# Performance work log

Measured on AMD Instinct MI355X. Metric: run time of the kernel, lower is better.

The kernel has to match this reference:

```python
import jax, jax.numpy as jnp
import numpy as np

B, T, IN, H, L, C = 64, 2048, 64, 128, 2, 8


def setup_inputs() -> dict:
    key = jax.random.key(0)
    ks = jax.random.split(key, 11)
    s = 1.0 / np.sqrt(H)  # torch nn.RNN default init scale
    return {
        "x": jax.random.normal(ks[0], (B, T, IN), dtype=jnp.float32),
        "W_ih0": jax.random.uniform(ks[1], (H, IN), jnp.float32, -s, s),
        "W_hh0": jax.random.uniform(ks[2], (H, H), jnp.float32, -s, s),
        "b_ih0": jax.random.uniform(ks[3], (H,), jnp.float32, -s, s),
        "b_hh0": jax.random.uniform(ks[4], (H,), jnp.float32, -s, s),
        "W_ih1": jax.random.uniform(ks[5], (H, H), jnp.float32, -s, s),
        "W_hh1": jax.random.uniform(ks[6], (H, H), jnp.float32, -s, s),
        "b_ih1": jax.random.uniform(ks[7], (H,), jnp.float32, -s, s),
        "b_hh1": jax.random.uniform(ks[8], (H,), jnp.float32, -s, s),
        "W_fc": jax.random.uniform(ks[9], (C, H), jnp.float32, -s, s),
        "b_fc": jax.random.uniform(ks[10], (C,), jnp.float32, -s, s),
    }


def _rnn_layer(x, W_ih, W_hh, b_ih, b_hh):
    # x: (B, T, D_in) -> (B, T, H); h0 = zeros (matches torch h0)
    # Precompute the input projection as one big GEMM outside the scan.
    x_proj = jnp.einsum('btd,hd->bth', x, W_ih) + b_ih + b_hh  # (B,T,H)
    x_proj_t = jnp.swapaxes(x_proj, 0, 1)  # (T,B,H)
    h0 = jnp.zeros((x.shape[0], W_hh.shape[0]), dtype=x.dtype)

    def step(h, xp):
        h_new = jnp.tanh(xp + h @ W_hh.T)
        return h_new, h_new

    _, hs = jax.lax.scan(step, h0, x_proj_t)  # (T,B,H)
    return jnp.swapaxes(hs, 0, 1)  # (B,T,H)


def reference(x, W_ih0, W_hh0, b_ih0, b_hh0, W_ih1, W_hh1, b_ih1, b_hh1, W_fc, b_fc):
    h1 = _rnn_layer(x, W_ih0, W_hh0, b_ih0, b_hh0)   # layer 0
    h2 = _rnn_layer(h1, W_ih1, W_hh1, b_ih1, b_hh1)  # layer 1
    logits = jnp.einsum('bth,ch->btc', h2, W_fc) + b_fc  # (B,T,C)
    return logits
```

## Files before the change

### kernel.cpp

```cpp
#include <hip/hip_runtime.h>

#define B_ 64
#define T_ 2048
#define IN_ 64
#define H_ 128
#define C_ 8

typedef _Float16 f16x2 __attribute__((ext_vector_type(2)));

__device__ __forceinline__ f16x2 pk(float a, float b) {
  f16x2 r; r.x = (_Float16)a; r.y = (_Float16)b; return r;
}
__device__ __forceinline__ f16x2 as_h2(int v) { return __builtin_bit_cast(f16x2, v); }

__device__ __forceinline__ float dot2(f16x2 a, f16x2 b, float c) {
#if __has_builtin(__builtin_amdgcn_fdot2)
  return __builtin_amdgcn_fdot2(a, b, c, false);
#else
  float r;
  asm("v_dot2_f32_f16 %0, %1, %2, %3" : "=v"(r) : "v"(a), "v"(b), "v"(c));
  return r;
#endif
}

__device__ __forceinline__ float tanh_fast(float x) {
  float e = __expf(2.0f * x);
  return 1.0f - 2.0f * __builtin_amdgcn_rcpf(e + 1.0f);
}

__device__ __forceinline__ float dpp_add_x1(float v) {
  return v + __int_as_float(__builtin_amdgcn_update_dpp(0, __float_as_int(v), 0xB1, 0xF, 0xF, true));
}
__device__ __forceinline__ float dpp_add_x2(float v) {
  return v + __int_as_float(__builtin_amdgcn_update_dpp(0, __float_as_int(v), 0x4E, 0xF, 0xF, true));
}
__device__ __forceinline__ float swz_add_x4(float v) {
  return v + __int_as_float(__builtin_amdgcn_ds_swizzle(__float_as_int(v), 0x101F));
}

__device__ __forceinline__ void block_sync_lds() {
  asm volatile("s_waitcnt lgkmcnt(0)" ::: "memory");
  __builtin_amdgcn_s_barrier();
  asm volatile("" ::: "memory");
}

#define DOT8(A, Q, W, BASE)            \
  A = dot2(as_h2(Q.x), W[BASE+0], A);  \
  A = dot2(as_h2(Q.y), W[BASE+1], A);  \
  A = dot2(as_h2(Q.z), W[BASE+2], A);  \
  A = dot2(as_h2(Q.w), W[BASE+3], A);

__global__ __launch_bounds__(256) void k_xproj(
    const float* __restrict__ x, const float* __restrict__ Wih0,
    const float* __restrict__ bih0, const float* __restrict__ bhh0,
    _Float16* __restrict__ xp) {
  __shared__ __align__(16) _Float16 xs[4][2][IN_];
  const int wave = threadIdx.x >> 6, lane = threadIdx.x & 63;
  const int gw = blockIdx.x * 4 + wave;
  const int ROWS = 32;
  const size_t r0 = (size_t)gw * ROWS;

  f16x2 wA[32], wB[32];
  const float2* W2 = (const float2*)Wih0;
#pragma unroll
  for (int p = 0; p < 32; ++p) {
    float2 a = W2[(lane * 2) * 32 + p];
    float2 b = W2[(lane * 2 + 1) * 32 + p];
    wA[p] = pk(a.x, a.y); wB[p] = pk(b.x, b.y);
  }
  const float ba = bih0[lane * 2] + bhh0[lane * 2];
  const float bb = bih0[lane * 2 + 1] + bhh0[lane * 2 + 1];

  xs[wave][0][lane] = (_Float16)x[r0 * IN_ + lane];
  float xn = x[(r0 + 1) * IN_ + lane];
  for (int rr = 0; rr < ROWS; ++rr) {
    const int buf = rr & 1;
    if (rr + 1 < ROWS) xs[wave][buf ^ 1][lane] = (_Float16)xn;
    if (rr + 2 < ROWS) xn = x[(r0 + rr + 2) * IN_ + lane];
    asm volatile("s_waitcnt lgkmcnt(0)" ::: "memory");
    const int4* xv = (const int4*)xs[wave][buf];
    int4 q0 = xv[0], q1 = xv[1], q2 = xv[2], q3 = xv[3];
    int4 q4 = xv[4], q5 = xv[5], q6 = xv[6], q7 = xv[7];
    float a0 = 0.f, a1 = 0.f, c0 = 0.f, c1 = 0.f;
    DOT8(a0, q0, wA, 0)  DOT8(c0, q0, wB, 0)
    DOT8(a1, q1, wA, 4)  DOT8(c1, q1, wB, 4)
    DOT8(a0, q2, wA, 8)  DOT8(c0, q2, wB, 8)
    DOT8(a1, q3, wA, 12) DOT8(c1, q3, wB, 12)
    DOT8(a0, q4, wA, 16) DOT8(c0, q4, wB, 16)
    DOT8(a1, q5, wA, 20) DOT8(c1, q5, wB, 20)
    DOT8(a0, q6, wA, 24) DOT8(c0, q6, wB, 24)
    DOT8(a1, q7, wA, 28) DOT8(c1, q7, wB, 28)
    *(f16x2*)&xp[(r0 + rr) * H_ + lane * 2] = pk(a0 + a1 + ba, c0 + c1 + bb);
  }
}

#define L0STEP(SS, XA, RI, WI)                                             \
  {                                                                        \
    block_sync_lds();                                                      \
    const int s_ = (SS);                                                   \
    if (s_ < T_) {                                                         \
      int4 q0 = hp[(RI) + rot0], q1 = hp[(RI) + rot1];                     \
      int4 q2 = hp[(RI) + rot2], q3 = hp[(RI) + rot3];                     \
      float a0 = 0.f, a1 = 0.f, c0 = 0.f, c1 = 0.f;                        \
      DOT8(a0, q0, wA, 0)  DOT8(c0, q0, wB, 0)                             \
      DOT8(a1, q1, wA, 4)  DOT8(c1, q1, wB, 4)                             \
      DOT8(a0, q2, wA, 8)  DOT8(c0, q2, wB, 8)                             \
      DOT8(a1, q3, wA, 12) DOT8(c1, q3, wB, 12)                            \
      float ra = dpp_add_x2(dpp_add_x1(a0 + a1));                          \
      float rc = dpp_add_x2(dpp_add_x1(c0 + c1));                          \
      float t0 = tanh_fast(ra + (float)XA.x);                              \
      float t1 = tanh_fast(rc + (float)XA.y);                              \
      const int sp = s_ + 4;                                               \
      if (sp < T_) XA = xp2[xpb + (size_t)sp * 64 + jx];                   \
      if (kq == 0) wp[(WI)] = pk(t0, t1);                                  \
    }                                                                      \
  }

#define L1STEP(SS, RI, WI)                                                 \
  {                                                                        \
    block_sync_lds();                                                      \
    const int s_ = (SS);                                                   \
    if (s_ >= 1 && s_ <= T_) {                                             \
      int4 q0 = hp[(RI) + rot0], q1 = hp[(RI) + rot1];                     \
      int4 q2 = hp[(RI) + rot2], q3 = hp[(RI) + rot3];                     \
      float a0 = 0.f, a1 = 0.f, c0 = 0.f, c1 = 0.f;                        \
      DOT8(a0, q0, vA, 0)  DOT8(c0, q0, vB, 0)                             \
      DOT8(a1, q1, vA, 4)  DOT8(c1, q1, vB, 4)                             \
      DOT8(a0, q2, vA, 8)  DOT8(c0, q2, vB, 8)                             \
      DOT8(a1, q3, vA, 12) DOT8(c1, q3, vB, 12)                            \
      float ra = swz_add_x4(dpp_add_x2(dpp_add_x1(a0 + a1)));              \
      float rc = swz_add_x4(dpp_add_x2(dpp_add_x1(c0 + c1)));              \
      float t0 = tanh_fast(ra + bA);                                       \
      float t1 = tanh_fast(rc + bB);                                       \
      if (ke == 0) wp[(WI)] = pk(t0, t1);                                  \
    }                                                                      \
  }

#define FCSTEP(SS, RI)                                                     \
  {                                                                        \
    block_sync_lds();                                                      \
    const int s_ = (SS);                                                   \
    if (s_ >= 2 && s_ < T_ + 2) {                                          \
      int4 q0 = hp[(RI)], q1 = hp[(RI) + 1];                               \
      float a0 = 0.f, a1 = 0.f;                                            \
      DOT8(a0, q0, wf, 0) DOT8(a1, q1, wf, 4)                              \
      float r = swz_add_x4(dpp_add_x2(dpp_add_x1(a0 + a1)));               \
      if (k8 == 0) outb[(size_t)(s_ - 2) * C_ + c] = r + bv;               \
    }                                                                      \
  }

__global__ __launch_bounds__(832) void k_rnn(
    const _Float16* __restrict__ xp0,
    const float* __restrict__ Whh0,
    const float* __restrict__ Wih1,
    const float* __restrict__ Whh1,
    const float* __restrict__ bih1,
    const float* __restrict__ bhh1,
    const float* __restrict__ Wfc,
    const float* __restrict__ bfc,
    float* __restrict__ out) {
  __shared__ __align__(16) _Float16 hlds[4][H_];

  const int tid  = threadIdx.x;
  const int wave = tid >> 6;
  const int lane = tid & 63;
  const int b    = blockIdx.x;

  if (tid < 256) ((int*)hlds)[tid] = 0;
  const int4*  hp = (const int4*)hlds;
  f16x2*       wp = (f16x2*)hlds;
  block_sync_lds();

  if (wave < 4) {
    const int jj = lane >> 2, kq = lane & 3;
    const int j0 = wave * 32 + jj * 2;
    const int rot0 = kq, rot1 = (1 + kq) & 3, rot2 = (2 + kq) & 3, rot3 = (3 + kq) & 3;
    f16x2 wA[16], wB[16];
    const float2* W2 = (const float2*)Whh0;
#pragma unroll
    for (int m = 0; m < 4; ++m) {
      const int cb = kq * 16 + (((m + kq) & 3)) * 4;
#pragma unroll
      for (int p = 0; p < 4; ++p) {
        float2 a = W2[j0 * 64 + cb + p];
        float2 bt = W2[(j0 + 1) * 64 + cb + p];
        wA[m * 4 + p] = pk(a.x, a.y);
        wB[m * 4 + p] = pk(bt.x, bt.y);
      }
    }
    const int riE = 16 + kq * 4, riO = kq * 4;
    const int wiE = (j0 >> 1), wiO = 64 + (j0 >> 1);
    const size_t xpb = (size_t)b * T_ * 64;
    const int jx = wave * 16 + jj;
    const f16x2* xp2 = (const f16x2*)xp0;
    f16x2 XA0 = xp2[xpb + 0 * 64 + jx], XA1 = xp2[xpb + 1 * 64 + jx];
    f16x2 XA2 = xp2[xpb + 2 * 64 + jx], XA3 = xp2[xpb + 3 * 64 + jx];
    for (int s0 = 0; s0 < T_ + 4; s0 += 4) {
      L0STEP(s0 + 0, XA0, riE, wiE)
      L0STEP(s0 + 1, XA1, riO, wiO)
      L0STEP(s0 + 2, XA2, riE, wiE)
      L0STEP(s0 + 3, XA3, riO, wiO)
    }
  } else if (wave < 12) {
    const int u = wave - 4;
    const int jj = lane >> 3, ke = lane & 7, kq = ke & 3;
    const int j0 = u * 16 + jj * 2;
    const int rot0 = kq, rot1 = (1 + kq) & 3, rot2 = (2 + kq) & 3, rot3 = (3 + kq) & 3;
    f16x2 vA[16], vB[16];
    const float2* W2 = (const float2*)(ke < 4 ? Wih1 : Whh1);
#pragma unroll
    for (int m = 0; m < 4; ++m) {
      const int cb = kq * 16 + (((m + kq) & 3)) * 4;
#pragma unroll
      for (int p = 0; p < 4; ++p) {
        float2 a = W2[j0 * 64 + cb + p];
        float2 bt = W2[(j0 + 1) * 64 + cb + p];
        vA[m * 4 + p] = pk(a.x, a.y);
        vB[m * 4 + p] = pk(bt.x, bt.y);
      }
    }
    const float bA = bih1[j0] + bhh1[j0];
    const float bB = bih1[j0 + 1] + bhh1[j0 + 1];
    const int riE = (ke < 4 ? 16 : 32) + kq * 4;
    const int riO = (ke < 4 ? 0 : 48) + kq * 4;
    const int wiE = 192 + (j0 >> 1), wiO = 128 + (j0 >> 1);
    for (int s = 0; s < T_ + 4; s += 2) {
      L1STEP(s,     riE, wiE)
      L1STEP(s + 1, riO, wiO)
    }
  } else {
    const int c = lane >> 3, k8 = lane & 7;
    f16x2 wf[8];
    const float2* W2 = (const float2*)Wfc;
#pragma unroll
    for (int p = 0; p < 8; ++p) {
      float2 a = W2[c * 64 + k8 * 8 + p];
      wf[p] = pk(a.x, a.y);
    }
    const float bv = bfc[c];
    float* outb = out + (size_t)b * T_ * C_;
    const int riE = 32 + k8 * 2, riO = 48 + k8 * 2;
    for (int s = 0; s < T_ + 4; s += 2) {
      FCSTEP(s,     riE)
      FCSTEP(s + 1, riO)
    }
  }
}

extern "C" void kernel_launch(void* const* d_in, const int* in_sizes, int n_in,
                              void* d_out, int out_size, void* d_ws, size_t ws_size,
                              hipStream_t stream) {
  const float* x    = (const float*)d_in[0];
  const float* Wih0 = (const float*)d_in[1];
  const float* Whh0 = (const float*)d_in[2];
  const float* bih0 = (const float*)d_in[3];
  const float* bhh0 = (const float*)d_in[4];
  const float* Wih1 = (const float*)d_in[5];
  const float* Whh1 = (const float*)d_in[6];
  const float* bih1 = (const float*)d_in[7];
  const float* bhh1 = (const float*)d_in[8];
  const float* Wfc  = (const float*)d_in[9];
  const float* bfc  = (const float*)d_in[10];
  float* outp = (float*)d_out;
  _Float16* xp0 = (_Float16*)d_ws;

  k_xproj<<<1024, 256, 0, stream>>>(x, Wih0, bih0, bhh0, xp0);
  k_rnn<<<64, 832, 0, stream>>>(xp0, Whh0, Wih1, Whh1, bih1, bhh1, Wfc, bfc, outp);
}
```

Baseline: 1.104 ms.

## Pipeline layer-1 input projection one step ahead and shorten reductions

Restructures the layer-1 waves so each lane handles both W_ih1 and W_hh1 for its column slice. The input-projection dot product for step t+1 is computed in the same phase as the recurrent update for step t, which takes the W_ih1 work off the serial critical path and lets the cross-lane reduction use only DPP ops (red8 with a row-shift) instead of ds_swizzle. Also drops the rotated LDS read pattern, uses exp2 directly in tanh, and limits x-projection loads to the writer lanes. This adds one more pipeline stage of latency (the FC output is shifted by three), and the new LDS access pattern without rotation may cause bank conflicts.

After: 1.108 ms. No clear change (+0.4%).

```diff
diff --git a/kernel.cpp b/kernel.cpp
--- a/kernel.cpp
+++ b/kernel.cpp
@@ -8,7 +8,10 @@
 
 typedef _Float16 f16x2 __attribute__((ext_vector_type(2)));
 
-__device__ __forceinline__ f16x2 pk(float a, float b) {
+__device__ __forceinline__ f16x2 pkw(float a, float b) {
+  return __builtin_bit_cast(f16x2, __builtin_amdgcn_cvt_pkrtz(a, b));
+}
+__device__ __forceinline__ f16x2 pk_rne(float a, float b) {
   f16x2 r; r.x = (_Float16)a; r.y = (_Float16)b; return r;
 }
 __device__ __forceinline__ f16x2 as_h2(int v) { return __builtin_bit_cast(f16x2, v); }
@@ -24,18 +27,20 @@
 }
 
 __device__ __forceinline__ float tanh_fast(float x) {
-  float e = __expf(2.0f * x);
+  float e = __builtin_amdgcn_exp2f(x * 2.8853900817779268f);
   return 1.0f - 2.0f * __builtin_amdgcn_rcpf(e + 1.0f);
 }
 
-__device__ __forceinline__ float dpp_add_x1(float v) {
-  return v + __int_as_float(__builtin_amdgcn_update_dpp(0, __float_as_int(v), 0xB1, 0xF, 0xF, true));
-}
-__device__ __forceinline__ float dpp_add_x2(float v) {
-  return v + __int_as_float(__builtin_amdgcn_update_dpp(0, __float_as_int(v), 0x4E, 0xF, 0xF, true));
-}
-__device__ __forceinline__ float swz_add_x4(float v) {
-  return v + __int_as_float(__builtin_amdgcn_ds_swizzle(__float_as_int(v), 0x101F));
+template <int CTRL>
+__device__ __forceinline__ float dpp_add(float v) {
+  return v + __int_as_float(__builtin_amdgcn_update_dpp(
+                 0, __float_as_int(v), CTRL, 0xF, 0xF, true));
+}
+__device__ __forceinline__ float red4(float v) {
+  return dpp_add<0x4E>(dpp_add<0xB1>(v));
+}
+__device__ __forceinline__ float red8(float v) {
+  return dpp_add<0x141>(dpp_add<0x4E>(dpp_add<0xB1>(v)));
 }
 
 __device__ __forceinline__ void block_sync_lds() {
@@ -66,7 +71,7 @@
   for (int p = 0; p < 32; ++p) {
     float2 a = W2[(lane * 2) * 32 + p];
     float2 b = W2[(lane * 2 + 1) * 32 + p];
-    wA[p] = pk(a.x, a.y); wB[p] = pk(b.x, b.y);
+    wA[p] = pkw(a.x, a.y); wB[p] = pkw(b.x, b.y);
   }
   const float ba = bih0[lane * 2] + bhh0[lane * 2];
   const float bb = bih0[lane * 2 + 1] + bhh0[lane * 2 + 1];
@@ -90,63 +95,67 @@
     DOT8(a1, q5, wA, 20) DOT8(c1, q5, wB, 20)
     DOT8(a0, q6, wA, 24) DOT8(c0, q6, wB, 24)
     DOT8(a1, q7, wA, 28) DOT8(c1, q7, wB, 28)
-    *(f16x2*)&xp[(r0 + rr) * H_ + lane * 2] = pk(a0 + a1 + ba, c0 + c1 + bb);
-  }
-}
-
-#define L0STEP(SS, XA, RI, WI)                                             \
-  {                                                                        \
-    block_sync_lds();                                                      \
-    const int s_ = (SS);                                                   \
-    if (s_ < T_) {                                                         \
-      int4 q0 = hp[(RI) + rot0], q1 = hp[(RI) + rot1];                     \
-      int4 q2 = hp[(RI) + rot2], q3 = hp[(RI) + rot3];                     \
-      float a0 = 0.f, a1 = 0.f, c0 = 0.f, c1 = 0.f;                        \
-      DOT8(a0, q0, wA, 0)  DOT8(c0, q0, wB, 0)                             \
-      DOT8(a1, q1, wA, 4)  DOT8(c1, q1, wB, 4)                             \
-      DOT8(a0, q2, wA, 8)  DOT8(c0, q2, wB, 8)                             \
-      DOT8(a1, q3, wA, 12) DOT8(c1, q3, wB, 12)                            \
-      float ra = dpp_add_x2(dpp_add_x1(a0 + a1));                          \
-      float rc = dpp_add_x2(dpp_add_x1(c0 + c1));                          \
-      float t0 = tanh_fast(ra + (float)XA.x);                              \
-      float t1 = tanh_fast(rc + (float)XA.y);                              \
-      const int sp = s_ + 4;                                               \
-      if (sp < T_) XA = xp2[xpb + (size_t)sp * 64 + jx];                   \
-      if (kq == 0) wp[(WI)] = pk(t0, t1);                                  \
-    }                                                                      \
-  }
-
-#define L1STEP(SS, RI, WI)                                                 \
-  {                                                                        \
-    block_sync_lds();                                                      \
-    const int s_ = (SS);                                                   \
-    if (s_ >= 1 && s_ <= T_) {                                             \
-      int4 q0 = hp[(RI) + rot0], q1 = hp[(RI) + rot1];                     \
-      int4 q2 = hp[(RI) + rot2], q3 = hp[(RI) + rot3];                     \
-      float a0 = 0.f, a1 = 0.f, c0 = 0.f, c1 = 0.f;                        \
-      DOT8(a0, q0, vA, 0)  DOT8(c0, q0, vB, 0)                             \
-      DOT8(a1, q1, vA, 4)  DOT8(c1, q1, vB, 4)                             \
-      DOT8(a0, q2, vA, 8)  DOT8(c0, q2, vB, 8)                             \
-      DOT8(a1, q3, vA, 12) DOT8(c1, q3, vB, 12)                            \
-      float ra = swz_add_x4(dpp_add_x2(dpp_add_x1(a0 + a1)));              \
-      float rc = swz_add_x4(dpp_add_x2(dpp_add_x1(c0 + c1)));              \
-      float t0 = tanh_fast(ra + bA);                                       \
-      float t1 = tanh_fast(rc + bB);                                       \
-      if (ke == 0) wp[(WI)] = pk(t0, t1);                                  \
-    }                                                                      \
-  }
-
-#define FCSTEP(SS, RI)                                                     \
-  {                                                                        \
-    block_sync_lds();                                                      \
-    const int s_ = (SS);                                                   \
-    if (s_ >= 2 && s_ < T_ + 2) {                                          \
-      int4 q0 = hp[(RI)], q1 = hp[(RI) + 1];                               \
-      float a0 = 0.f, a1 = 0.f;                                            \
-      DOT8(a0, q0, wf, 0) DOT8(a1, q1, wf, 4)                              \
-      float r = swz_add_x4(dpp_add_x2(dpp_add_x1(a0 + a1)));               \
-      if (k8 == 0) outb[(size_t)(s_ - 2) * C_ + c] = r + bv;               \
-    }                                                                      \
+    *(f16x2*)&xp[(r0 + rr) * H_ + lane * 2] = pk_rne(a0 + a1 + ba, c0 + c1 + bb);
+  }
+}
+
+
+#define L0PH(PP, XA, RB, WPB)                                          \
+  {                                                                    \
+    block_sync_lds();                                                  \
+    const int p_ = (PP);                                               \
+    if (p_ < T_) {                                                     \
+      const float fx = (float)XA.x, fy = (float)XA.y;                  \
+      int4 q0 = hp[(RB) + kq4 + 0], q1 = hp[(RB) + kq4 + 1];           \
+      int4 q2 = hp[(RB) + kq4 + 2], q3 = hp[(RB) + kq4 + 3];           \
+      float a0 = 0.f, a1 = 0.f, c0 = 0.f, c1 = 0.f;                    \
+      DOT8(a0, q0, wA, 0)  DOT8(c0, q0, wB, 0)                         \
+      DOT8(a1, q1, wA, 4)  DOT8(c1, q1, wB, 4)                         \
+      DOT8(a0, q2, wA, 8)  DOT8(c0, q2, wB, 8)                         \
+      DOT8(a1, q3, wA, 12) DOT8(c1, q3, wB, 12)                        \
+      float t0 = tanh_fast(red4(a0 + a1) + fx);                        \
+      float t1 = tanh_fast(red4(c0 + c1) + fy);                        \
+      if (kq == 0) {                                                   \
+        wp[(WPB) + jx] = pk_rne(t0, t1);                               \
+        const int pp = p_ + 4;                                         \
+        if (pp < T_) XA = xp2[xpb + (size_t)pp * 64 + jx];             \
+      }                                                                \
+    }                                                                  \
+  }
+
+#define L1PH(PP, RH2, WPB, RH1)                                        \
+  {                                                                    \
+    block_sync_lds();                                                  \
+    const int p_ = (PP);                                               \
+    if (p_ >= 2 && p_ < T_ + 2) {                                      \
+      int4 h0 = hp[(RH2) + kg2], h1v = hp[(RH2) + kg2 + 1];            \
+      float a = pi0, c = pi1;                                          \
+      DOT8(a, h0, whA, 0) DOT8(a, h1v, whA, 4)                         \
+      DOT8(c, h0, whB, 0) DOT8(c, h1v, whB, 4)                         \
+      float t0 = tanh_fast(red8(a) + bA);                              \
+      float t1 = tanh_fast(red8(c) + bB);                              \
+      if (kg == 0) wp[(WPB) + jy] = pk_rne(t0, t1);                    \
+    }                                                                  \
+    if (p_ <= T_) {                                                    \
+      int4 g0 = hp[(RH1) + kg2], g1 = hp[(RH1) + kg2 + 1];             \
+      float x0 = 0.f, x1 = 0.f;                                        \
+      DOT8(x0, g0, wiA, 0) DOT8(x0, g1, wiA, 4)                        \
+      DOT8(x1, g0, wiB, 0) DOT8(x1, g1, wiB, 4)                        \
+      pi0 = x0; pi1 = x1;                                              \
+    }                                                                  \
+  }
+
+#define FCPH(PP, RB)                                                   \
+  {                                                                    \
+    block_sync_lds();                                                  \
+    const int p_ = (PP);                                               \
+    if (p_ >= 3 && p_ < T_ + 3) {                                      \
+      int4 h0 = hp[(RB) + kg2], h1v = hp[(RB) + kg2 + 1];              \
+      float a = 0.f;                                                   \
+      DOT8(a, h0, wf, 0) DOT8(a, h1v, wf, 4)                           \
+      float r = red8(a);                                               \
+      if (k8 == 0) outb[(size_t)(p_ - 3) * C_ + cc] = r + bv;          \
+    }                                                                  \
   }
 
 __global__ __launch_bounds__(832) void k_rnn(
@@ -167,82 +176,77 @@
   const int b    = blockIdx.x;
 
   if (tid < 256) ((int*)hlds)[tid] = 0;
-  const int4*  hp = (const int4*)hlds;
-  f16x2*       wp = (f16x2*)hlds;
+  const int4* hp = (const int4*)hlds;
+  f16x2*      wp = (f16x2*)hlds;
   block_sync_lds();
 
   if (wave < 4) {
     const int jj = lane >> 2, kq = lane & 3;
+    const int kq4 = kq * 4;
     const int j0 = wave * 32 + jj * 2;
-    const int rot0 = kq, rot1 = (1 + kq) & 3, rot2 = (2 + kq) & 3, rot3 = (3 + kq) & 3;
+    const int jx = wave * 16 + jj;
     f16x2 wA[16], wB[16];
     const float2* W2 = (const float2*)Whh0;
 #pragma unroll
-    for (int m = 0; m < 4; ++m) {
-      const int cb = kq * 16 + (((m + kq) & 3)) * 4;
-#pragma unroll
-      for (int p = 0; p < 4; ++p) {
-        float2 a = W2[j0 * 64 + cb + p];
-        float2 bt = W2[(j0 + 1) * 64 + cb + p];
-        wA[m * 4 + p] = pk(a.x, a.y);
-        wB[m * 4 + p] = pk(bt.x, bt.y);
+    for (int m = 0; m < 4; ++m)
+#pragma unroll
+      for (int e = 0; e < 4; ++e) {
+        float2 a = W2[j0 * 64 + kq * 16 + m * 4 + e];
+        float2 bt = W2[(j0 + 1) * 64 + kq * 16 + m * 4 + e];
+        wA[m * 4 + e] = pkw(a.x, a.y);
+        wB[m * 4 + e] = pkw(bt.x, bt.y);
       }
-    }
-    const int riE = 16 + kq * 4, riO = kq * 4;
-    const int wiE = (j0 >> 1), wiO = 64 + (j0 >> 1);
     const size_t xpb = (size_t)b * T_ * 64;
-    const int jx = wave * 16 + jj;
     const f16x2* xp2 = (const f16x2*)xp0;
-    f16x2 XA0 = xp2[xpb + 0 * 64 + jx], XA1 = xp2[xpb + 1 * 64 + jx];
-    f16x2 XA2 = xp2[xpb + 2 * 64 + jx], XA3 = xp2[xpb + 3 * 64 + jx];
-    for (int s0 = 0; s0 < T_ + 4; s0 += 4) {
-      L0STEP(s0 + 0, XA0, riE, wiE)
-      L0STEP(s0 + 1, XA1, riO, wiO)
-      L0STEP(s0 + 2, XA2, riE, wiE)
-      L0STEP(s0 + 3, XA3, riO, wiO)
+    f16x2 XA0 = {0,0}, XA1 = {0,0}, XA2 = {0,0}, XA3 = {0,0};
+    if (kq == 0) {
+      XA0 = xp2[xpb + 0 * 64 + jx]; XA1 = xp2[xpb + 1 * 64 + jx];
+      XA2 = xp2[xpb + 2 * 64 + jx]; XA3 = xp2[xpb + 3 * 64 + jx];
+    }
+    for (int p0 = 0; p0 < T_ + 4; p0 += 4) {
+      L0PH(p0 + 0, XA0, 16, 0)
+      L0PH(p0 + 1, XA1, 0, 64)
+      L0PH(p0 + 2, XA2, 16, 0)
+      L0PH(p0 + 3, XA3, 0, 64)
     }
   } else if (wave < 12) {
     const int u = wave - 4;
-    const int jj = lane >> 3, ke = lane & 7, kq = ke & 3;
+    const int jj = lane >> 3, kg = lane & 7;
+    const int kg2 = kg * 2;
     const int j0 = u * 16 + jj * 2;
-    const int rot0 = kq, rot1 = (1 + kq) & 3, rot2 = (2 + kq) & 3, rot3 = (3 + kq) & 3;
-    f16x2 vA[16], vB[16];
-    const float2* W2 = (const float2*)(ke < 4 ? Wih1 : Whh1);
-#pragma unroll
-    for (int m = 0; m < 4; ++m) {
-      const int cb = kq * 16 + (((m + kq) & 3)) * 4;
-#pragma unroll
-      for (int p = 0; p < 4; ++p) {
-        float2 a = W2[j0 * 64 + cb + p];
-        float2 bt = W2[(j0 + 1) * 64 + cb + p];
-        vA[m * 4 + p] = pk(a.x, a.y);
-        vB[m * 4 + p] = pk(bt.x, bt.y);
-      }
+    const int jy = u * 8 + jj;
+    f16x2 whA[8], whB[8], wiA[8], wiB[8];
+    const float2* Wh2 = (const float2*)Whh1;
+    const float2* Wi2 = (const float2*)Wih1;
+#pragma unroll
+    for (int n = 0; n < 8; ++n) {
+      float2 a = Wi2[j0 * 64 + kg * 8 + n];        wiA[n] = pkw(a.x, a.y);
+      float2 bq = Wi2[(j0 + 1) * 64 + kg * 8 + n]; wiB[n] = pkw(bq.x, bq.y);
+      float2 cq = Wh2[j0 * 64 + kg * 8 + n];       whA[n] = pkw(cq.x, cq.y);
+      float2 dq = Wh2[(j0 + 1) * 64 + kg * 8 + n]; whB[n] = pkw(dq.x, dq.y);
     }
     const float bA = bih1[j0] + bhh1[j0];
     const float bB = bih1[j0 + 1] + bhh1[j0 + 1];
-    const int riE = (ke < 4 ? 16 : 32) + kq * 4;
-    const int riO = (ke < 4 ? 0 : 48) + kq * 4;
-    const int wiE = 192 + (j0 >> 1), wiO = 128 + (j0 >> 1);
-    for (int s = 0; s < T_ + 4; s += 2) {
-      L1STEP(s,     riE, wiE)
-      L1STEP(s + 1, riO, wiO)
+    float pi0 = 0.f, pi1 = 0.f;
+    for (int p0 = 0; p0 < T_ + 4; p0 += 2) {
+      L1PH(p0 + 0, 48, 128, 16)
+      L1PH(p0 + 1, 32, 192, 0)
     }
   } else {
-    const int c = lane >> 3, k8 = lane & 7;
+    const int cc = lane >> 3, k8 = lane & 7;
+    const int kg2 = k8 * 2;
     f16x2 wf[8];
     const float2* W2 = (const float2*)Wfc;
 #pragma unroll
-    for (int p = 0; p < 8; ++p) {
-      float2 a = W2[c * 64 + k8 * 8 + p];
-      wf[p] = pk(a.x, a.y);
-    }
-    const float bv = bfc[c];
+    for (int n = 0; n < 8; ++n) {
+      float2 a = W2[cc * 64 + k8 * 8 + n];
+      wf[n] = pkw(a.x, a.y);
+    }
+    const float bv = bfc[cc];
     float* outb = out + (size_t)b * T_ * C_;
-    const int riE = 32 + k8 * 2, riO = 48 + k8 * 2;
-    for (int s = 0; s < T_ + 4; s += 2) {
-      FCSTEP(s,     riE)
-      FCSTEP(s + 1, riO)
+    for (int p0 = 0; p0 < T_ + 4; p0 += 2) {
+      FCPH(p0 + 0, 48)
+      FCPH(p0 + 1, 32)
     }
   }
 }
```
